# Optimization experiments

Hardware: AMD Instinct MI355X
Metric: run time of the kernel (lower is better)

The kernel has to match this reference:

```python
import jax, jax.numpy as jnp
import numpy as np

NEG = -1e6  # mask fill value used by d2l.sequence_mask


def setup_inputs() -> dict:
    key = jax.random.key(0)
    k1, k2, k3, k4, k5, k6, k7 = jax.random.split(key, 7)
    B, Q, K, DQ, DK, H, DV = 8, 256, 1024, 256, 256, 128, 128
    queries = jax.random.normal(k1, (B, Q, DQ), dtype=jnp.float32)
    keys = jax.random.normal(k2, (B, K, DK), dtype=jnp.float32)
    values = jax.random.normal(k3, (B, K, DV), dtype=jnp.float32)
    valid_lens = jax.random.randint(k4, (B,), 1, K + 1, dtype=jnp.int32)
    # learned params (nn.Linear stores weight as [out, in]; apply as x @ W.T)
    W_q = jax.random.normal(k5, (H, DQ), dtype=jnp.float32) / np.sqrt(DQ)
    W_k = jax.random.normal(k6, (H, DK), dtype=jnp.float32) / np.sqrt(DK)
    w_v = jax.random.normal(k7, (H,), dtype=jnp.float32) / np.sqrt(H)
    return {"queries": queries, "keys": keys, "values": values,
            "valid_lens": valid_lens, "W_q": W_q, "W_k": W_k, "w_v": w_v}


def reference(queries, keys, values, valid_lens, W_q, W_k, w_v):
    # projections
    q = jnp.einsum('bqd,hd->bqh', queries, W_q)   # [B,Q,H]
    k = jnp.einsum('bkd,hd->bkh', keys, W_k)      # [B,K,H]
    # broadcast add + tanh -> [B,Q,K,H] (the fusion-headroom intermediate)
    features = jnp.tanh(q[:, :, None, :] + k[:, None, :, :])
    scores = jnp.einsum('bqkh,h->bqk', features, w_v)  # [B,Q,K]
    # masked softmax: valid_lens is per-batch (dim==1 path)
    klen = scores.shape[-1]
    mask = jnp.arange(klen)[None, None, :] < valid_lens[:, None, None]
    scores = jnp.where(mask, scores, NEG)
    weights = jax.nn.softmax(scores, axis=-1)
    # dropout is identity in eval mode
    return jnp.einsum('bqk,bkv->bqv', weights, values)
```

## Files before the change

### kernel.cpp

```cpp
#include <hip/hip_runtime.h>


#define Bb 8
#define Qn 256
#define Kk 1024
#define Dd 256
#define Hh 128
#define DVv 128

__device__ __forceinline__ float fexp2(float x) { return __builtin_amdgcn_exp2f(x); }
__device__ __forceinline__ float frcp(float x)  { return __builtin_amdgcn_rcpf(x); }

__global__ __launch_bounds__(256)
void repack_w(const float* __restrict__ Wq, const float* __restrict__ Wk,
              float4* __restrict__ Wq4T, float4* __restrict__ Wk4T)
{
    const int blk = blockIdx.x;
    const float* src = (blk < 32) ? Wq : Wk;
    float4*      dst = (blk < 32) ? Wq4T : Wk4T;
    const int idx = (blk & 31) * 256 + threadIdx.x;
    const int g = idx >> 7;
    const int h = idx & 127;
    dst[idx] = *(const float4*)(src + (size_t)h * Dd + g * 4);
}

__global__ __launch_bounds__(512)
void proj_exp_kernel(const float* __restrict__ queries,
                     const float* __restrict__ keys,
                     const float4* __restrict__ Wq4T,
                     const float4* __restrict__ Wk4T,
                     float* __restrict__ EqT,
                     float* __restrict__ EkT)
{
    __shared__ __align__(16) float Xs[16 * 256];
    const int blk = blockIdx.x;
    const float* X; const float4* W4; float* outT; int RB; int i0;
    if (blk < 128) { X = queries; W4 = Wq4T; outT = EqT; RB = Qn; i0 = blk * 16; }
    else           { X = keys;    W4 = Wk4T; outT = EkT; RB = Kk; i0 = (blk - 128) * 16; }
    const int tid = threadIdx.x;
    const int h   = tid & 127;
    const int r4  = __builtin_amdgcn_readfirstlane(tid >> 7);

    {
        const float4* xsrc = (const float4*)(X + (size_t)i0 * Dd);
#pragma unroll
        for (int s = 0; s < 2; ++s) {
            const int idx = tid + 512 * s;
            *(float4*)(Xs + idx * 4) = xsrc[idx];
        }
    }
    __syncthreads();

    float acc[4] = {0.f, 0.f, 0.f, 0.f};
    const float4* wp = W4 + h;
    const float*  xr = Xs + (r4 * 4) * 256;
#pragma unroll 8
    for (int g = 0; g < 64; ++g) {
        const float4 w = wp[(size_t)g * 128];
#pragma unroll
        for (int i = 0; i < 4; ++i) {
            const float4 x = *(const float4*)(xr + i * 256 + g * 4);
            acc[i] = fmaf(x.x, w.x, acc[i]);
            acc[i] = fmaf(x.y, w.y, acc[i]);
            acc[i] = fmaf(x.z, w.z, acc[i]);
            acc[i] = fmaf(x.w, w.w, acc[i]);
        }
    }
    const int b    = i0 / RB;
    const int rloc = (i0 % RB) + r4 * 4;
    float4 o;
    o.x = fexp2(acc[0] * 2.885390082f);
    o.y = fexp2(acc[1] * 2.885390082f);
    o.z = fexp2(acc[2] * 2.885390082f);
    o.w = fexp2(acc[3] * 2.885390082f);
    *(float4*)(outT + (size_t)b * Hh * RB + (size_t)h * RB + rloc) = o;
}

__global__ __launch_bounds__(1024, 8)
void score_softmax_pv_kernel(const float* __restrict__ EqT,
                             const float* __restrict__ EkT,
                             const float* __restrict__ wv,
                             const int* __restrict__ valid_lens,
                             const float* __restrict__ values,
                             float* __restrict__ out)
{
    __shared__ __align__(16) float  s_sc[4][Kk];
    __shared__ __align__(16) float  eqsT[4][Hh];
    __shared__ __align__(16) float  w2s[Hh];
    __shared__ __align__(16) float4 s_part[15][4][32];
    __shared__ float s_qmax[4][4];
    __shared__ float s_qsum[4][4];

    const int blk  = blockIdx.x;
    const int qt   = blk >> 3;
    const int b    = (blk & 7) ^ ((qt & 32) ? 4 : 0);
    const int q0   = qt * 4;
    const int len  = valid_lens[b];
    const int tid  = threadIdx.x;
    const int lane = tid & 63;
    const int wave = __builtin_amdgcn_readfirstlane(tid >> 6);

    if (tid < 128) {
        const float4 v = *(const float4*)(EqT + (size_t)b * Hh * Qn + (size_t)tid * Qn + q0);
        eqsT[0][tid] = v.x; eqsT[1][tid] = v.y; eqsT[2][tid] = v.z; eqsT[3][tid] = v.w;
    } else if (tid < 256) {
        w2s[tid - 128] = -2.0f * wv[tid - 128];
    }
    ((float4*)s_sc)[tid] = make_float4(0.f, 0.f, 0.f, 0.f);
    __syncthreads();

    const int qh = __builtin_amdgcn_readfirstlane(tid >> 8);
    const int kg = tid & 255;
    const int kw = ((tid >> 6) & 3) * 256;

    if (kw < len) {
        const float4* ek4 = (const float4*)(EkT + (size_t)b * Hh * Kk) + kg;
        const int h0 = qh << 5;
        float acc[4][4] = {};
#pragma unroll 1
        for (int hg = 0; hg < 8; ++hg) {
            const int h = h0 + (hg << 2);
            const float4 e0 = ek4[(h + 0) * (Kk / 4)];
            const float4 e1 = ek4[(h + 1) * (Kk / 4)];
            const float4 e2 = ek4[(h + 2) * (Kk / 4)];
            const float4 e3 = ek4[(h + 3) * (Kk / 4)];
            const float4 w4 = *(const float4*)(w2s + h);
#pragma unroll
            for (int q = 0; q < 4; ++q) {
                const float4 q4 = *(const float4*)(&eqsT[q][h]);
                {
                    const float A = fmaf(q4.x, e0.x, 1.f), B = fmaf(q4.y, e1.x, 1.f);
                    const float C = fmaf(q4.z, e2.x, 1.f), E = fmaf(q4.w, e3.x, 1.f);
                    const float AB = A * B, CE = C * E;
                    const float N = fmaf(fmaf(w4.x, B, w4.y * A), CE,
                                         fmaf(w4.z, E, w4.w * C) * AB);
                    acc[q][0] = fmaf(N, frcp(AB * CE), acc[q][0]);
                }
                {
                    const float A = fmaf(q4.x, e0.y, 1.f), B = fmaf(q4.y, e1.y, 1.f);
                    const float C = fmaf(q4.z, e2.y, 1.f), E = fmaf(q4.w, e3.y, 1.f);
                    const float AB = A * B, CE = C * E;
                    const float N = fmaf(fmaf(w4.x, B, w4.y * A), CE,
                                         fmaf(w4.z, E, w4.w * C) * AB);
                    acc[q][1] = fmaf(N, frcp(AB * CE), acc[q][1]);
                }
                {
                    const float A = fmaf(q4.x, e0.z, 1.f), B = fmaf(q4.y, e1.z, 1.f);
                    const float C = fmaf(q4.z, e2.z, 1.f), E = fmaf(q4.w, e3.z, 1.f);
                    const float AB = A * B, CE = C * E;
                    const float N = fmaf(fmaf(w4.x, B, w4.y * A), CE,
                                         fmaf(w4.z, E, w4.w * C) * AB);
                    acc[q][2] = fmaf(N, frcp(AB * CE), acc[q][2]);
                }
                {
                    const float A = fmaf(q4.x, e0.w, 1.f), B = fmaf(q4.y, e1.w, 1.f);
                    const float C = fmaf(q4.z, e2.w, 1.f), E = fmaf(q4.w, e3.w, 1.f);
                    const float AB = A * B, CE = C * E;
                    const float N = fmaf(fmaf(w4.x, B, w4.y * A), CE,
                                         fmaf(w4.z, E, w4.w * C) * AB);
                    acc[q][3] = fmaf(N, frcp(AB * CE), acc[q][3]);
                }
            }
        }
#pragma unroll
        for (int q = 0; q < 4; ++q)
#pragma unroll
            for (int kk = 0; kk < 4; ++kk)
                atomicAdd(&s_sc[q][(kg << 2) + kk], acc[q][kk]);
    }
    __syncthreads();

    {
        const int q    = wave & 3;
        const int qtr  = wave >> 2;
        const int base = qtr * 256;
        const int hi   = (base + 256 < len) ? base + 256 : len;
        float m = -3.0e38f;
        for (int i = base + lane; i < hi; i += 64) m = fmaxf(m, s_sc[q][i]);
#pragma unroll
        for (int off = 32; off > 0; off >>= 1) m = fmaxf(m, __shfl_xor(m, off));
        if (lane == 0) s_qmax[q][qtr] = m;
        __syncthreads();
        const float gm = fmaxf(fmaxf(s_qmax[q][0], s_qmax[q][1]),
                               fmaxf(s_qmax[q][2], s_qmax[q][3]));
        float sum = 0.f;
        for (int i = base + lane; i < hi; i += 64) {
            const float p = fexp2((s_sc[q][i] - gm) * 1.44269504f);
            s_sc[q][i] = p;
            sum += p;
        }
#pragma unroll
        for (int off = 32; off > 0; off >>= 1) sum += __shfl_xor(sum, off);
        if (lane == 0) s_qsum[q][qtr] = sum;
    }
    __syncthreads();

    {
        const int slice = tid >> 5;
        const int l32   = tid & 31;
        const int v4    = l32 << 2;
        const float* vp = values + (size_t)b * Kk * DVv + v4;
        float a[4][4];
#pragma unroll
        for (int q = 0; q < 4; ++q) { a[q][0]=0.f; a[q][1]=0.f; a[q][2]=0.f; a[q][3]=0.f; }
        for (int k = slice; k < len; k += 32) {
            const float4 val = *(const float4*)(vp + (size_t)k * DVv);
            const float w0 = s_sc[0][k], w1 = s_sc[1][k], w2 = s_sc[2][k], w3 = s_sc[3][k];
            a[0][0] = fmaf(w0, val.x, a[0][0]);
            a[0][1] = fmaf(w0, val.y, a[0][1]);
            a[0][2] = fmaf(w0, val.z, a[0][2]);
            a[0][3] = fmaf(w0, val.w, a[0][3]);
            a[1][0] = fmaf(w1, val.x, a[1][0]);
            a[1][1] = fmaf(w1, val.y, a[1][1]);
            a[1][2] = fmaf(w1, val.z, a[1][2]);
            a[1][3] = fmaf(w1, val.w, a[1][3]);
            a[2][0] = fmaf(w2, val.x, a[2][0]);
            a[2][1] = fmaf(w2, val.y, a[2][1]);
            a[2][2] = fmaf(w2, val.z, a[2][2]);
            a[2][3] = fmaf(w2, val.w, a[2][3]);
            a[3][0] = fmaf(w3, val.x, a[3][0]);
            a[3][1] = fmaf(w3, val.y, a[3][1]);
            a[3][2] = fmaf(w3, val.z, a[3][2]);
            a[3][3] = fmaf(w3, val.w, a[3][3]);
        }
#pragma unroll
        for (int q = 0; q < 4; ++q)
#pragma unroll
            for (int x = 0; x < 4; ++x) a[q][x] += __shfl_xor(a[q][x], 32);
        if (wave > 0 && lane < 32) {
#pragma unroll
            for (int q = 0; q < 4; ++q)
                s_part[wave - 1][q][l32] = make_float4(a[q][0], a[q][1], a[q][2], a[q][3]);
        }
        __syncthreads();
        if (wave == 0 && lane < 32) {
#pragma unroll
            for (int q = 0; q < 4; ++q) {
                float r0 = a[q][0], r1 = a[q][1], r2 = a[q][2], r3 = a[q][3];
#pragma unroll
                for (int w = 0; w < 15; ++w) {
                    const float4 p = s_part[w][q][l32];
                    r0 += p.x; r1 += p.y; r2 += p.z; r3 += p.w;
                }
                const float inv = frcp(s_qsum[q][0] + s_qsum[q][1] +
                                       s_qsum[q][2] + s_qsum[q][3]);
                *(float4*)(out + (size_t)(b * Qn + q0 + q) * DVv + v4) =
                    make_float4(r0 * inv, r1 * inv, r2 * inv, r3 * inv);
            }
        }
    }
}

extern "C" void kernel_launch(void* const* d_in, const int* in_sizes, int n_in,
                              void* d_out, int out_size, void* d_ws, size_t ws_size,
                              hipStream_t stream) {
    (void)in_sizes; (void)n_in; (void)out_size; (void)ws_size;
    const float* queries    = (const float*)d_in[0];
    const float* keys       = (const float*)d_in[1];
    const float* values     = (const float*)d_in[2];
    const int*   valid_lens = (const int*)  d_in[3];
    const float* Wq         = (const float*)d_in[4];
    const float* Wk         = (const float*)d_in[5];
    const float* wvv        = (const float*)d_in[6];
    float* out = (float*)d_out;

    float* Wq4T = (float*)d_ws;
    float* Wk4T = Wq4T + (size_t)Dd * Hh;
    float* EqT  = Wk4T + (size_t)Dd * Hh;
    float* EkT  = EqT + (size_t)Bb * Hh * Qn;

    repack_w       <<<  64, 256, 0, stream>>>(Wq, Wk, (float4*)Wq4T, (float4*)Wk4T);
    proj_exp_kernel<<< 640, 512, 0, stream>>>(queries, keys, (const float4*)Wq4T,
                                              (const float4*)Wk4T, EqT, EkT);
    score_softmax_pv_kernel<<<512, 1024, 0, stream>>>(EqT, EkT, wvv, valid_lens,
                                                      values, out);
}
```

Baseline: 144.3 us.

## Halve score block to 512 threads, each thread owning two keys across all H

The score/softmax/PV kernel now runs 512-thread blocks. Each thread handles 2 keys over the full hidden dimension, where before 4 threads split H into quarters and reduced with LDS atomicAdd. This removes the shared-memory atomics and the zeroing of the score buffer. The softmax and PV reductions are rescaled to 8 waves, and the batch swizzle of block indices is dropped. In exchange each thread does more serial work and there are fewer threads per block, which could cut latency hiding.

```diff
diff --git a/kernel.cpp b/kernel.cpp
--- a/kernel.cpp
+++ b/kernel.cpp
@@ -76,7 +76,7 @@
     *(float4*)(outT + (size_t)b * Hh * RB + (size_t)h * RB + rloc) = o;
 }
 
-__global__ __launch_bounds__(1024, 8)
+__global__ __launch_bounds__(512, 8)
 void score_softmax_pv_kernel(const float* __restrict__ EqT,
                              const float* __restrict__ EkT,
                              const float* __restrict__ wv,
@@ -87,13 +87,13 @@
     __shared__ __align__(16) float  s_sc[4][Kk];
     __shared__ __align__(16) float  eqsT[4][Hh];
     __shared__ __align__(16) float  w2s[Hh];
-    __shared__ __align__(16) float4 s_part[15][4][32];
-    __shared__ float s_qmax[4][4];
-    __shared__ float s_qsum[4][4];
+    __shared__ __align__(16) float4 s_part[7][4][32];
+    __shared__ float s_qmax[4][2];
+    __shared__ float s_qsum[4][2];
 
     const int blk  = blockIdx.x;
+    const int b    = blk & 7;
     const int qt   = blk >> 3;
-    const int b    = (blk & 7) ^ ((qt & 32) ? 4 : 0);
     const int q0   = qt * 4;
     const int len  = valid_lens[b];
     const int tid  = threadIdx.x;
@@ -106,24 +106,19 @@
     } else if (tid < 256) {
         w2s[tid - 128] = -2.0f * wv[tid - 128];
     }
-    ((float4*)s_sc)[tid] = make_float4(0.f, 0.f, 0.f, 0.f);
-    __syncthreads();
-
-    const int qh = __builtin_amdgcn_readfirstlane(tid >> 8);
-    const int kg = tid & 255;
-    const int kw = ((tid >> 6) & 3) * 256;
-
-    if (kw < len) {
-        const float4* ek4 = (const float4*)(EkT + (size_t)b * Hh * Kk) + kg;
-        const int h0 = qh << 5;
-        float acc[4][4] = {};
-#pragma unroll 1
-        for (int hg = 0; hg < 8; ++hg) {
-            const int h = h0 + (hg << 2);
-            const float4 e0 = ek4[(h + 0) * (Kk / 4)];
-            const float4 e1 = ek4[(h + 1) * (Kk / 4)];
-            const float4 e2 = ek4[(h + 2) * (Kk / 4)];
-            const float4 e3 = ek4[(h + 3) * (Kk / 4)];
+    __syncthreads();
+
+    const int kspan = (tid >> 6) << 7;
+    if (kspan < len) {
+        const float2* ek2 = (const float2*)(EkT + (size_t)b * Hh * Kk) + tid;
+        float acc[4][2] = {};
+#pragma unroll 2
+        for (int hg = 0; hg < 32; ++hg) {
+            const int h = hg << 2;
+            const float2 e0 = ek2[(size_t)(h + 0) * (Kk / 2)];
+            const float2 e1 = ek2[(size_t)(h + 1) * (Kk / 2)];
+            const float2 e2 = ek2[(size_t)(h + 2) * (Kk / 2)];
+            const float2 e3 = ek2[(size_t)(h + 3) * (Kk / 2)];
             const float4 w4 = *(const float4*)(w2s + h);
 #pragma unroll
             for (int q = 0; q < 4; ++q) {
@@ -144,45 +139,26 @@
                                          fmaf(w4.z, E, w4.w * C) * AB);
                     acc[q][1] = fmaf(N, frcp(AB * CE), acc[q][1]);
                 }
-                {
-                    const float A = fmaf(q4.x, e0.z, 1.f), B = fmaf(q4.y, e1.z, 1.f);
-                    const float C = fmaf(q4.z, e2.z, 1.f), E = fmaf(q4.w, e3.z, 1.f);
-                    const float AB = A * B, CE = C * E;
-                    const float N = fmaf(fmaf(w4.x, B, w4.y * A), CE,
-                                         fmaf(w4.z, E, w4.w * C) * AB);
-                    acc[q][2] = fmaf(N, frcp(AB * CE), acc[q][2]);
-                }
-                {
-                    const float A = fmaf(q4.x, e0.w, 1.f), B = fmaf(q4.y, e1.w, 1.f);
-                    const float C = fmaf(q4.z, e2.w, 1.f), E = fmaf(q4.w, e3.w, 1.f);
-                    const float AB = A * B, CE = C * E;
-                    const float N = fmaf(fmaf(w4.x, B, w4.y * A), CE,
-                                         fmaf(w4.z, E, w4.w * C) * AB);
-                    acc[q][3] = fmaf(N, frcp(AB * CE), acc[q][3]);
-                }
             }
         }
 #pragma unroll
         for (int q = 0; q < 4; ++q)
-#pragma unroll
-            for (int kk = 0; kk < 4; ++kk)
-                atomicAdd(&s_sc[q][(kg << 2) + kk], acc[q][kk]);
+            *(float2*)(&s_sc[q][tid << 1]) = make_float2(acc[q][0], acc[q][1]);
     }
     __syncthreads();
 
     {
         const int q    = wave & 3;
-        const int qtr  = wave >> 2;
-        const int base = qtr * 256;
-        const int hi   = (base + 256 < len) ? base + 256 : len;
+        const int half = wave >> 2;
+        const int base = half * 512;
+        const int hi   = (base + 512 < len) ? base + 512 : len;
         float m = -3.0e38f;
         for (int i = base + lane; i < hi; i += 64) m = fmaxf(m, s_sc[q][i]);
 #pragma unroll
         for (int off = 32; off > 0; off >>= 1) m = fmaxf(m, __shfl_xor(m, off));
-        if (lane == 0) s_qmax[q][qtr] = m;
+        if (lane == 0) s_qmax[q][half] = m;
         __syncthreads();
-        const float gm = fmaxf(fmaxf(s_qmax[q][0], s_qmax[q][1]),
-                               fmaxf(s_qmax[q][2], s_qmax[q][3]));
+        const float gm = fmaxf(s_qmax[q][0], s_qmax[q][1]);
         float sum = 0.f;
         for (int i = base + lane; i < hi; i += 64) {
             const float p = fexp2((s_sc[q][i] - gm) * 1.44269504f);
@@ -191,7 +167,7 @@
         }
 #pragma unroll
         for (int off = 32; off > 0; off >>= 1) sum += __shfl_xor(sum, off);
-        if (lane == 0) s_qsum[q][qtr] = sum;
+        if (lane == 0) s_qsum[q][half] = sum;
     }
     __syncthreads();
 
@@ -203,7 +179,7 @@
         float a[4][4];
 #pragma unroll
         for (int q = 0; q < 4; ++q) { a[q][0]=0.f; a[q][1]=0.f; a[q][2]=0.f; a[q][3]=0.f; }
-        for (int k = slice; k < len; k += 32) {
+        for (int k = slice; k < len; k += 16) {
             const float4 val = *(const float4*)(vp + (size_t)k * DVv);
             const float w0 = s_sc[0][k], w1 = s_sc[1][k], w2 = s_sc[2][k], w3 = s_sc[3][k];
             a[0][0] = fmaf(w0, val.x, a[0][0]);
@@ -238,12 +214,11 @@
             for (int q = 0; q < 4; ++q) {
                 float r0 = a[q][0], r1 = a[q][1], r2 = a[q][2], r3 = a[q][3];
 #pragma unroll
-                for (int w = 0; w < 15; ++w) {
+                for (int w = 0; w < 7; ++w) {
                     const float4 p = s_part[w][q][l32];
                     r0 += p.x; r1 += p.y; r2 += p.z; r3 += p.w;
                 }
-                const float inv = frcp(s_qsum[q][0] + s_qsum[q][1] +
-                                       s_qsum[q][2] + s_qsum[q][3]);
+                const float inv = frcp(s_qsum[q][0] + s_qsum[q][1]);
                 *(float4*)(out + (size_t)(b * Qn + q0 + q) * DVv + v4) =
                     make_float4(r0 * inv, r1 * inv, r2 * inv, r3 * inv);
             }
@@ -272,6 +247,6 @@
     repack_w       <<<  64, 256, 0, stream>>>(Wq, Wk, (float4*)Wq4T, (float4*)Wk4T);
     proj_exp_kernel<<< 640, 512, 0, stream>>>(queries, keys, (const float4*)Wq4T,
                                               (const float4*)Wk4T, EqT, EkT);
-    score_softmax_pv_kernel<<<512, 1024, 0, stream>>>(EqT, EkT, wvv, valid_lens,
-                                                      values, out);
-}
+    score_softmax_pv_kernel<<<512, 512, 0, stream>>>(EqT, EkT, wvv, valid_lens,
+                                                     values, out);
+}
```

Result: faster. 134.4 us (-6.8%).
